# Kernel tuning notes

Measured on AMD Instinct MI355X. Metric: run time of the kernel, lower is better.

## Reference

```python
import jax, jax.numpy as jnp
import numpy as np

N = 50000      # num nodes
E = 800000     # num edges (before self loops)
B = 50         # num graphs in batch
F_IN = 15
C = 64         # hidden_channels
H = 4          # num_heads
NEG_SLOPE = 0.2  # PyG GATConv default


def setup_inputs() -> dict:
    key = jax.random.key(0)
    ks = jax.random.split(key, 32)
    s = 0.05
    inp = {
        "x": jax.random.normal(ks[0], (N, F_IN), dtype=jnp.float32),
        "edge_index": jax.random.randint(ks[1], (2, E), 0, N, dtype=jnp.int32),
        "batch": jnp.sort(jax.random.randint(ks[2], (N,), 0, B, dtype=jnp.int32)),
        "W1": jax.random.normal(ks[3], (F_IN, H * C)) * s,
        "aS1": jax.random.normal(ks[4], (H, C)) * s,
        "aD1": jax.random.normal(ks[5], (H, C)) * s,
        "b1": jnp.zeros((H * C,)),
        "W2": jax.random.normal(ks[6], (H * C, H * C)) * s,
        "aS2": jax.random.normal(ks[7], (H, C)) * s,
        "aD2": jax.random.normal(ks[8], (H, C)) * s,
        "b2": jnp.zeros((H * C,)),
        # GAT layer 3: 256 -> 64, 1 head
        "W3": jax.random.normal(ks[9], (H * C, C)) * s,
        "aS3": jax.random.normal(ks[10], (1, C)) * s,
        "aD3": jax.random.normal(ks[11], (1, C)) * s,
        "b3": jnp.zeros((C,)),
        # node attention MLP: 64 -> 32 -> 1
        "Wna1": jax.random.normal(ks[12], (C, 32)) * s,
        "bna1": jnp.zeros((32,)),
        "Wna2": jax.random.normal(ks[13], (32, 1)) * s,
        "bna2": jnp.zeros((1,)),
        # graph classifier: 128 -> 128 -> 64 -> 1
        "Wc1": jax.random.normal(ks[14], (2 * C, 128)) * s,
        "bc1": jnp.zeros((128,)),
        "Wc2": jax.random.normal(ks[15], (128, 64)) * s,
        "bc2": jnp.zeros((64,)),
        "Wc3": jax.random.normal(ks[16], (64, 1)) * s,
        "bc3": jnp.zeros((1,)),
    }
    return inp


def _gat_conv(x, src, dst, W, a_src, a_dst, b, heads, ch):
    """PyG-style GATConv (add_self_loops=True, negative_slope=0.2, eval mode)."""
    n = x.shape[0]
    h = (x @ W).reshape(n, heads, ch)               # [N, H, C]
    alpha_s = jnp.einsum('nhc,hc->nh', h, a_src)    # per-node src score
    alpha_d = jnp.einsum('nhc,hc->nh', h, a_dst)
    loops = jnp.arange(n, dtype=src.dtype)
    s = jnp.concatenate([src, loops])               # [E+N]
    d = jnp.concatenate([dst, loops])
    e = jax.nn.leaky_relu(alpha_s[s] + alpha_d[d], NEG_SLOPE)   # [E+N, H]
    # segment softmax over incoming edges of each dst node
    m = jax.ops.segment_max(e, d, num_segments=n)
    ex = jnp.exp(e - m[d])
    denom = jax.ops.segment_sum(ex, d, num_segments=n)
    alpha = ex / denom[d]                           # [E+N, H]
    msg = h[s] * alpha[:, :, None]                  # [E+N, H, C]
    out = jax.ops.segment_sum(msg, d, num_segments=n)  # [N, H, C]
    return out.reshape(n, heads * ch) + b


def reference(x, edge_index, batch, W1, aS1, aD1, b1, W2, aS2, aD2, b2,
              W3, aS3, aD3, b3, Wna1, bna1, Wna2, bna2,
              Wc1, bc1, Wc2, bc2, Wc3, bc3):
    src, dst = edge_index[0], edge_index[1]
    x1 = jax.nn.elu(_gat_conv(x, src, dst, W1, aS1, aD1, b1, H, C))
    x2 = jax.nn.elu(_gat_conv(x1, src, dst, W2, aS2, aD2, b2, H, C))
    x3 = jax.nn.elu(_gat_conv(x2, src, dst, W3, aS3, aD3, b3, 1, C))  # [N, 64]

    # node attention: MLP then softmax over ALL nodes (dim=0, as in source)
    na = jax.nn.relu(x3 @ Wna1 + bna1) @ Wna2 + bna2   # [N, 1]
    node_attention = jax.nn.softmax(na, axis=0)

    # graph pooling
    ones = jnp.ones((x3.shape[0],), dtype=x3.dtype)
    cnt = jax.ops.segment_sum(ones, batch, num_segments=B)         # [B]
    mean = jax.ops.segment_sum(x3, batch, num_segments=B) / jnp.maximum(cnt, 1.0)[:, None]
    mx = jax.ops.segment_max(x3, batch, num_segments=B)
    mx = jnp.where(cnt[:, None] > 0, mx, 0.0)
    g = jnp.concatenate([mean, mx], axis=1)                        # [B, 128]

    h1 = jax.nn.relu(g @ Wc1 + bc1)
    h2 = jax.nn.relu(h1 @ Wc2 + bc2)
    risk = jax.nn.sigmoid(h2 @ Wc3 + bc3)                          # [B, 1]
    return (risk, node_attention)
```

## Files before the change

kernel.cpp:

```cpp
#include <hip/hip_runtime.h>
#include <math.h>

#define NN 50000
#define NP 50176
#define EE 800000
#define ETOT (EE + NN)
#define BB 50
#define PC 16

typedef unsigned short u16;
typedef unsigned char u8;
typedef __attribute__((ext_vector_type(8))) short short8;
typedef __attribute__((ext_vector_type(8))) unsigned short ushort8;
typedef __attribute__((ext_vector_type(4))) float floatx4;
typedef __attribute__((ext_vector_type(2))) float floatx2;

__device__ __forceinline__ float b2f(u16 u) {
  return __int_as_float(((int)u) << 16);
}
__device__ __forceinline__ u16 f2b(float f) {
  unsigned u = __float_as_uint(f);
  unsigned r = (u + 0x7fffu + ((u >> 16) & 1u)) >> 16;
  return (u16)r;
}
__device__ __forceinline__ u8 f2f8(float v) {
  return (u8)(__builtin_amdgcn_cvt_pk_fp8_f32(v, v, 0, false) & 0xFF);
}
__device__ __forceinline__ float readlane_f(float v, int l) {
  return __int_as_float(__builtin_amdgcn_readlane(__float_as_int(v), l));
}

__global__ void count_kernel(const int* __restrict__ ei, int* __restrict__ cnt) {
  int e = blockIdx.x * blockDim.x + threadIdx.x;
  if (e >= ETOT) return;
  int d = (e < EE) ? ei[EE + e] : (e - EE);
  atomicAdd(&cnt[d], 1);
}

__global__ void scan1_kernel(const int* __restrict__ cnt, int* __restrict__ rowp,
                             int* __restrict__ part) {
  __shared__ int s[512];
  int t = threadIdx.x;
  int i = blockIdx.x * 512 + t;
  int v = (i < NN) ? cnt[i] : 0;
  s[t] = v;
  __syncthreads();
  for (int off = 1; off < 512; off <<= 1) {
    int add = (t >= off) ? s[t - off] : 0;
    __syncthreads();
    s[t] += add;
    __syncthreads();
  }
  if (i < NN) rowp[i] = s[t] - v;
  if (t == 511) part[blockIdx.x] = s[511];
}

__global__ void scan2_kernel(int* __restrict__ part, int* __restrict__ rowp) {
  __shared__ int s[128];
  int t = threadIdx.x;
  int v = (t < 98) ? part[t] : 0;
  s[t] = v;
  __syncthreads();
  for (int off = 1; off < 128; off <<= 1) {
    int add = (t >= off) ? s[t - off] : 0;
    __syncthreads();
    s[t] += add;
    __syncthreads();
  }
  if (t < 98) part[t] = s[t] - v;
  if (t == 97) rowp[NN] = s[97];
}

__global__ void scan3_kernel(int* __restrict__ rowp, const int* __restrict__ part) {
  int i = blockIdx.x * 512 + threadIdx.x;
  if (i < NN) rowp[i] += part[blockIdx.x];
}

__global__ void fill_kernel(const int* __restrict__ ei, const int* __restrict__ rowp,
                            int* __restrict__ cur, int* __restrict__ col) {
  int e = blockIdx.x * blockDim.x + threadIdx.x;
  if (e >= ETOT) return;
  int s, d;
  if (e < EE) { s = ei[e]; d = ei[EE + e]; } else { s = e - EE; d = s; }
  int p = atomicAdd(&cur[d], 1);
  col[rowp[d] + p] = s;
}

__global__ void prep_kernel(const float* __restrict__ x, const float* __restrict__ W1,
                            const float* __restrict__ W2, const float* __restrict__ W3,
                            u16* __restrict__ xb, u16* __restrict__ W1t,
                            u16* __restrict__ W2t, u16* __restrict__ W3t) {
  const int T0 = NP * 32, T1 = T0 + 8192, T2 = T1 + 65536, T3 = T2 + 16384;
  int i = blockIdx.x * 256 + threadIdx.x;
  if (i < T0) {
    int n = i >> 5, c = i & 31;
    xb[i] = (n < NN && c < 15) ? f2b(x[n * 15 + c]) : (u16)0;
  } else if (i < T1) {
    int j = i - T0, n = j >> 5, k = j & 31;
    W1t[j] = (k < 15) ? f2b(W1[k * 256 + n]) : (u16)0;
  } else if (i < T2) {
    int j = i - T1, n = j >> 8, k = j & 255;
    W2t[j] = f2b(W2[k * 256 + n]);
  } else if (i < T3) {
    int j = i - T2, n = j >> 8, k = j & 255;
    W3t[j] = f2b(W3[k * 64 + n]);
  }
}

template <int BK>
__global__ __launch_bounds__(256) void gemm128_kernel(
    const u16* __restrict__ A, const u16* __restrict__ Bt, u8* __restrict__ C8,
    int K, const float* __restrict__ aS, const float* __restrict__ aD,
    float* __restrict__ as_o, float* __restrict__ ad_o) {
  __shared__ u16 Al[128][BK + 8];
  __shared__ u16 Bl[128][BK + 8];
  int R0 = blockIdx.x * 128, C0 = blockIdx.y * 128;
  int wid = threadIdx.x >> 6, lane = threadIdx.x & 63;
  int wr = (wid >> 1) * 64, wc = (wid & 1) * 64;
  int lrow = lane & 15, lk8 = (lane >> 4) * 8;
  int rq = (lane >> 4) * 4;
  const int Q8 = BK / 8;
  const int nA8 = 128 * Q8;
  floatx4 acc[4][4];
#pragma unroll
  for (int i = 0; i < 4; ++i)
#pragma unroll
    for (int j = 0; j < 4; ++j) acc[i][j] = (floatx4){0.f, 0.f, 0.f, 0.f};

  for (int k0 = 0; k0 < K; k0 += BK) {
    for (int c = threadIdx.x; c < 2 * nA8; c += 256) {
      if (c < nA8) {
        int r = c / Q8, o = (c % Q8) * 8;
        *(ushort8*)&Al[r][o] = *(const ushort8*)&A[(size_t)(R0 + r) * K + k0 + o];
      } else {
        int c2 = c - nA8;
        int r = c2 / Q8, o = (c2 % Q8) * 8;
        *(ushort8*)&Bl[r][o] = *(const ushort8*)&Bt[(size_t)(C0 + r) * K + k0 + o];
      }
    }
    __syncthreads();
#pragma unroll
    for (int ks = 0; ks < BK / 32; ++ks) {
      short8 a[4], b[4];
#pragma unroll
      for (int i = 0; i < 4; ++i) a[i] = *(const short8*)&Al[wr + i * 16 + lrow][ks * 32 + lk8];
#pragma unroll
      for (int j = 0; j < 4; ++j) b[j] = *(const short8*)&Bl[wc + j * 16 + lrow][ks * 32 + lk8];
#pragma unroll
      for (int i = 0; i < 4; ++i)
#pragma unroll
        for (int j = 0; j < 4; ++j)
          acc[i][j] = __builtin_amdgcn_mfma_f32_16x16x32_bf16(a[i], b[j], acc[i][j], 0, 0, 0);
    }
    __syncthreads();
  }
#pragma unroll
  for (int i = 0; i < 4; ++i)
#pragma unroll
    for (int j = 0; j < 4; ++j)
#pragma unroll
      for (int q = 0; q < 4; ++q) {
        int gr = R0 + wr + i * 16 + rq + q;
        int gc = C0 + wc + j * 16 + lrow;
        C8[(size_t)gr * 256 + gc] = f2f8(acc[i][j][q]);
      }
  int hb = blockIdx.y * 2 + (wid & 1);
  float wS[4], wD[4];
#pragma unroll
  for (int j = 0; j < 4; ++j) {
    wS[j] = aS[hb * 64 + j * 16 + lrow];
    wD[j] = aD[hb * 64 + j * 16 + lrow];
  }
#pragma unroll
  for (int i = 0; i < 4; ++i)
#pragma unroll
    for (int q = 0; q < 4; ++q) {
      float vS = acc[i][0][q] * wS[0] + acc[i][1][q] * wS[1] +
                 acc[i][2][q] * wS[2] + acc[i][3][q] * wS[3];
      float vD = acc[i][0][q] * wD[0] + acc[i][1][q] * wD[1] +
                 acc[i][2][q] * wD[2] + acc[i][3][q] * wD[3];
#pragma unroll
      for (int o = 8; o; o >>= 1) {
        vS += __shfl_xor(vS, o, 64);
        vD += __shfl_xor(vD, o, 64);
      }
      if (lrow == 0) {
        int gr = R0 + wr + i * 16 + rq + q;
        as_o[(size_t)gr * 4 + hb] = vS;
        ad_o[(size_t)gr * 4 + hb] = vD;
      }
    }
}

__global__ __launch_bounds__(256) void gemm64_kernel(
    const u16* __restrict__ A, const u16* __restrict__ Bt, u16* __restrict__ C,
    int K, const float* __restrict__ aS, const float* __restrict__ aD,
    float* __restrict__ as_o, float* __restrict__ ad_o) {
  const int BK = 64;
  __shared__ u16 Al[128][BK + 8];
  __shared__ u16 Bl[64][BK + 8];
  __shared__ float sS[4][64], sD[4][64];
  int R0 = blockIdx.x * 128;
  int wid = threadIdx.x >> 6, lane = threadIdx.x & 63;
  int wr = (wid >> 1) * 64, wc = (wid & 1) * 32;
  int lrow = lane & 15, lk8 = (lane >> 4) * 8;
  int rq = (lane >> 4) * 4;
  const int Q4 = BK / 4;
  const int nA = 128 * Q4, nB = 64 * Q4;
  floatx4 acc[4][2];
#pragma unroll
  for (int i = 0; i < 4; ++i)
#pragma unroll
    for (int j = 0; j < 2; ++j) acc[i][j] = (floatx4){0.f, 0.f, 0.f, 0.f};

  for (int k0 = 0; k0 < K; k0 += BK) {
    for (int c = threadIdx.x; c < nA + nB; c += 256) {
      if (c < nA) {
        int r = c / Q4, o = (c % Q4) * 4;
        *(ushort4*)&Al[r][o] = *(const ushort4*)&A[(size_t)(R0 + r) * K + k0 + o];
      } else {
        int c2 = c - nA;
        int r = c2 / Q4, o = (c2 % Q4) * 4;
        *(ushort4*)&Bl[r][o] = *(const ushort4*)&Bt[(size_t)r * K + k0 + o];
      }
    }
    __syncthreads();
#pragma unroll
    for (int ks = 0; ks < BK / 32; ++ks) {
      short8 a[4], b[2];
#pragma unroll
      for (int i = 0; i < 4; ++i) a[i] = *(const short8*)&Al[wr + i * 16 + lrow][ks * 32 + lk8];
#pragma unroll
      for (int j = 0; j < 2; ++j) b[j] = *(const short8*)&Bl[wc + j * 16 + lrow][ks * 32 + lk8];
#pragma unroll
      for (int i = 0; i < 4; ++i)
#pragma unroll
        for (int j = 0; j < 2; ++j)
          acc[i][j] = __builtin_amdgcn_mfma_f32_16x16x32_bf16(a[i], b[j], acc[i][j], 0, 0, 0);
    }
    __syncthreads();
  }
#pragma unroll
  for (int i = 0; i < 4; ++i)
#pragma unroll
    for (int j = 0; j < 2; ++j)
#pragma unroll
      for (int q = 0; q < 4; ++q) {
        int gr = R0 + wr + i * 16 + rq + q;
        C[(size_t)gr * 64 + wc + j * 16 + lrow] = f2b(acc[i][j][q]);
      }
  float wS0 = aS[wc + lrow], wS1 = aS[wc + 16 + lrow];
  float wD0 = aD[wc + lrow], wD1 = aD[wc + 16 + lrow];
#pragma unroll
  for (int i = 0; i < 4; ++i)
#pragma unroll
    for (int q = 0; q < 4; ++q) {
      float vS = acc[i][0][q] * wS0 + acc[i][1][q] * wS1;
      float vD = acc[i][0][q] * wD0 + acc[i][1][q] * wD1;
#pragma unroll
      for (int o = 8; o; o >>= 1) {
        vS += __shfl_xor(vS, o, 64);
        vD += __shfl_xor(vD, o, 64);
      }
      if (lrow == 0) {
        int rl = i * 16 + rq + q;
        sS[wid][rl] = vS;
        sD[wid][rl] = vD;
      }
    }
  __syncthreads();
  if (threadIdx.x < 128) {
    int p = threadIdx.x >> 6, r = threadIdx.x & 63;
    int gr = R0 + p * 64 + r;
    as_o[gr] = sS[2 * p][r] + sS[2 * p + 1][r];
    ad_o[gr] = sD[2 * p][r] + sD[2 * p + 1][r];
  }
}

template <int LAYER>
__global__ __launch_bounds__(256) void escore4_kernel(
    const float* __restrict__ as_i, const float* __restrict__ ad_i,
    const int* __restrict__ rowp, const int* __restrict__ col,
    float4* __restrict__ exl) {
  int wid = threadIdx.x >> 6, lane = threadIdx.x & 63;
  int d = blockIdx.x * 4 + wid;
  int rp0 = rowp[d], rp1 = rowp[d + 1];
  float4 add = *(const float4*)&ad_i[(size_t)d * 4];
  for (int i = rp0 + lane; i < rp1; i += 64) {
    int s = col[i];
    float4 a = *(const float4*)&as_i[(size_t)s * 4];
    float e0 = a.x + add.x, e1 = a.y + add.y, e2 = a.z + add.z, e3 = a.w + add.w;
    e0 = (e0 > 0.f) ? e0 : 0.2f * e0;
    e1 = (e1 > 0.f) ? e1 : 0.2f * e1;
    e2 = (e2 > 0.f) ? e2 : 0.2f * e2;
    e3 = (e3 > 0.f) ? e3 : 0.2f * e3;
    exl[i] = make_float4(__expf(e0), __expf(e1), __expf(e2), __expf(e3));
  }
}

__global__ __launch_bounds__(256) void escore1_kernel(
    const float* __restrict__ as_i, const float* __restrict__ ad_i,
    const int* __restrict__ rowp, const int* __restrict__ col,
    float* __restrict__ exl) {
  int wid = threadIdx.x >> 6, lane = threadIdx.x & 63;
  int d = blockIdx.x * 4 + wid;
  int rp0 = rowp[d], rp1 = rowp[d + 1];
  float add = ad_i[d];
  for (int i = rp0 + lane; i < rp1; i += 64) {
    float e = as_i[col[i]] + add;
    e = (e > 0.f) ? e : 0.2f * e;
    exl[i] = __expf(e);
  }
}

template <int LAYER>
__global__ __launch_bounds__(256) void agg4_kernel(
    const u8* __restrict__ h8, const float4* __restrict__ exl,
    const int* __restrict__ rowp, const int* __restrict__ col,
    const float* __restrict__ bias, u16* __restrict__ xo) {
  __shared__ float exs[4][64][4];
  int wid = threadIdx.x >> 6, lane = threadIdx.x & 63;
  int d = blockIdx.x * 4 + wid;
  int rp0 = rowp[d], deg = rowp[d + 1] - rp0;
  int hj = lane >> 4;
  int lq = lane << 2;
  float a0 = 0.f, a1 = 0.f, a2 = 0.f, a3 = 0.f;
  float den0 = 0.f, den1 = 0.f, den2 = 0.f, den3 = 0.f;

  for (int base = 0; base < deg; base += 64) {
    int i = base + lane;
    bool valid = i < deg;
    int s = valid ? col[rp0 + i] : 0;
    float4 xv = valid ? exl[rp0 + i] : make_float4(0.f, 0.f, 0.f, 0.f);
    den0 += xv.x; den1 += xv.y; den2 += xv.z; den3 += xv.w;
    *(float4*)&exs[wid][lane][0] = xv;
    __threadfence_block();
    int cnt = min(64, deg - base);
    int k8 = cnt & ~7;
    for (int k = 0; k < k8; k += 8) {
      unsigned wv[8];
      float qv[8];
#pragma unroll
      for (int u = 0; u < 8; ++u) {
        int sk = __builtin_amdgcn_readlane(s, k + u);
        qv[u] = exs[wid][k + u][hj];
        wv[u] = *(const unsigned*)&h8[(size_t)sk * 256 + lq];
      }
#pragma unroll
      for (int u = 0; u < 8; ++u) {
        floatx2 lo = __builtin_amdgcn_cvt_pk_f32_fp8(wv[u], false);
        floatx2 hi = __builtin_amdgcn_cvt_pk_f32_fp8(wv[u], true);
        a0 += qv[u] * lo.x;
        a1 += qv[u] * lo.y;
        a2 += qv[u] * hi.x;
        a3 += qv[u] * hi.y;
      }
    }
    for (int k = k8; k < cnt; ++k) {
      int sk = __builtin_amdgcn_readlane(s, k);
      float qk = exs[wid][k][hj];
      unsigned wv = *(const unsigned*)&h8[(size_t)sk * 256 + lq];
      floatx2 lo = __builtin_amdgcn_cvt_pk_f32_fp8(wv, false);
      floatx2 hi = __builtin_amdgcn_cvt_pk_f32_fp8(wv, true);
      a0 += qk * lo.x;
      a1 += qk * lo.y;
      a2 += qk * hi.x;
      a3 += qk * hi.y;
    }
  }
#pragma unroll
  for (int o = 32; o; o >>= 1) {
    den0 += __shfl_xor(den0, o, 64);
    den1 += __shfl_xor(den1, o, 64);
    den2 += __shfl_xor(den2, o, 64);
    den3 += __shfl_xor(den3, o, 64);
  }
  float den = (hj == 0) ? den0 : (hj == 1) ? den1 : (hj == 2) ? den2 : den3;
  float inv = 1.f / den;
  float4 bv = *(const float4*)&bias[lq];
  float v0 = a0 * inv + bv.x;
  float v1 = a1 * inv + bv.y;
  float v2 = a2 * inv + bv.z;
  float v3 = a3 * inv + bv.w;
  v0 = (v0 > 0.f) ? v0 : expm1f(v0);
  v1 = (v1 > 0.f) ? v1 : expm1f(v1);
  v2 = (v2 > 0.f) ? v2 : expm1f(v2);
  v3 = (v3 > 0.f) ? v3 : expm1f(v3);
  ushort4 o4;
  o4.x = f2b(v0); o4.y = f2b(v1); o4.z = f2b(v2); o4.w = f2b(v3);
  ((ushort4*)xo)[(size_t)d * 64 + lane] = o4;
}

__global__ __launch_bounds__(256) void agg1na_kernel(
    const u16* __restrict__ h, const float* __restrict__ exl,
    const int* __restrict__ rowp, const int* __restrict__ col,
    const float* __restrict__ bias, float* __restrict__ xo,
    const float* __restrict__ Wna1, const float* __restrict__ bna1,
    const float* __restrict__ Wna2, const float* __restrict__ bna2,
    float* __restrict__ na) {
  __shared__ float Ws[2048];
  __shared__ float W2s[32];
  __shared__ float xrow[4][64];
  for (int i = threadIdx.x; i < 2048; i += 256) Ws[i] = Wna1[i];
  if (threadIdx.x < 32) W2s[threadIdx.x] = Wna2[threadIdx.x];
  __syncthreads();
  int wid = threadIdx.x >> 6, lane = threadIdx.x & 63;
  int d = blockIdx.x * 4 + wid;
  int rp0 = rowp[d], deg = rowp[d + 1] - rp0;
  float acc = 0.f, den = 0.f;
  for (int base = 0; base < deg; base += 64) {
    int i = base + lane;
    bool valid = i < deg;
    int s = valid ? col[rp0 + i] : 0;
    float ex = valid ? exl[rp0 + i] : 0.f;
    den += ex;
    int cnt = min(64, deg - base);
    int k8 = cnt & ~7;
    for (int k = 0; k < k8; k += 8) {
      int sA[8];
      float qA[8], hv[8];
#pragma unroll
      for (int u = 0; u < 8; ++u) {
        sA[u] = __builtin_amdgcn_readlane(s, k + u);
        qA[u] = readlane_f(ex, k + u);
      }
#pragma unroll
      for (int u = 0; u < 8; ++u) hv[u] = b2f(h[(size_t)sA[u] * 64 + lane]);
      float p0 = qA[0] * hv[0] + qA[1] * hv[1];
      float p1 = qA[2] * hv[2] + qA[3] * hv[3];
      float p2 = qA[4] * hv[4] + qA[5] * hv[5];
      float p3 = qA[6] * hv[6] + qA[7] * hv[7];
      acc += (p0 + p1) + (p2 + p3);
    }
    for (int k = k8; k < cnt; ++k) {
      int sk = __builtin_amdgcn_readlane(s, k);
      float qk = readlane_f(ex, k);
      acc += qk * b2f(h[(size_t)sk * 64 + lane]);
    }
  }
#pragma unroll
  for (int o = 32; o; o >>= 1) den += __shfl_xor(den, o, 64);
  float v = acc / den + bias[lane];
  v = (v > 0.f) ? v : expm1f(v);
  xo[(size_t)d * 64 + lane] = v;
  xrow[wid][lane] = v;
  __threadfence_block();
  int j = lane & 31;
  int coff = (lane >> 5) * 32;
  float hj = 0.f;
#pragma unroll
  for (int c = 0; c < 32; ++c) hj += xrow[wid][coff + c] * Ws[(coff + c) * 32 + j];
  hj += __shfl_xor(hj, 32, 64);
  hj += bna1[j];
  float r = fmaxf(hj, 0.f) * W2s[j];
#pragma unroll
  for (int o = 16; o; o >>= 1) r += __shfl_xor(r, o, 64);
  if (lane == 0) na[d] = __expf(r + bna2[0]);
}

__global__ void na_sum_kernel(const float* __restrict__ na, float* __restrict__ gsum) {
  __shared__ float s[4];
  float acc = 0.f;
  for (int i = blockIdx.x * blockDim.x + threadIdx.x; i < NN; i += gridDim.x * blockDim.x)
    acc += na[i];
  for (int o = 32; o; o >>= 1) acc += __shfl_xor(acc, o, 64);
  int wid = threadIdx.x >> 6, lane = threadIdx.x & 63;
  if (lane == 0) s[wid] = acc;
  __syncthreads();
  if (threadIdx.x == 0) atomicAdd(gsum, s[0] + s[1] + s[2] + s[3]);
}

__global__ void na_write_kernel(const float* __restrict__ na, const float* __restrict__ gsum,
                                float* __restrict__ out) {
  int n = blockIdx.x * blockDim.x + threadIdx.x;
  if (n >= NN) return;
  out[n] = na[n] / gsum[0];
}

__global__ void pool1_kernel(const float* __restrict__ x3, const int* __restrict__ batch,
                             float* __restrict__ ppsum, float* __restrict__ ppmax) {
  int b = blockIdx.x, c = blockIdx.y;
  int lane = threadIdx.x & 63, wid = threadIdx.x >> 6;
  int lo = 0, hi = NN;
  while (lo < hi) { int m = (lo + hi) >> 1; if (batch[m] < b) lo = m + 1; else hi = m; }
  int start = lo;
  lo = start; hi = NN;
  while (lo < hi) { int m = (lo + hi) >> 1; if (batch[m] < b + 1) lo = m + 1; else hi = m; }
  int end = lo;
  int len = end - start;
  int c0 = start + (int)((long)len * c / PC);
  int c1 = start + (int)((long)len * (c + 1) / PC);
  float acc = 0.f, mx = -INFINITY;
  for (int n = c0 + wid; n < c1; n += 4) {
    float v = x3[(size_t)n * 64 + lane];
    acc += v;
    mx = fmaxf(mx, v);
  }
  __shared__ float ssum[4][64], smax[4][64];
  ssum[wid][lane] = acc;
  smax[wid][lane] = mx;
  __syncthreads();
  if (wid == 0) {
    acc = ssum[0][lane] + ssum[1][lane] + ssum[2][lane] + ssum[3][lane];
    mx = fmaxf(fmaxf(smax[0][lane], smax[1][lane]), fmaxf(smax[2][lane], smax[3][lane]));
    size_t o = ((size_t)c * BB + b) * 64 + lane;
    ppsum[o] = acc;
    ppmax[o] = mx;
  }
}

__global__ void pool2cls_kernel(const float* __restrict__ ppsum, const float* __restrict__ ppmax,
                                const int* __restrict__ batch, const float* __restrict__ Wc1,
                                const float* __restrict__ bc1, const float* __restrict__ Wc2,
                                const float* __restrict__ bc2, const float* __restrict__ Wc3,
                                const float* __restrict__ bc3, float* __restrict__ out) {
  __shared__ float g[128], h1[128], h2[64], scnt;
  int b = blockIdx.x, t = threadIdx.x;
  if (t == 0) {
    int lo = 0, hi = NN;
    while (lo < hi) { int m = (lo + hi) >> 1; if (batch[m] < b) lo = m + 1; else hi = m; }
    int start = lo;
    lo = start; hi = NN;
    while (lo < hi) { int m = (lo + hi) >> 1; if (batch[m] < b + 1) lo = m + 1; else hi = m; }
    scnt = (float)(lo - start);
  }
  float s = 0.f, m = -INFINITY;
  if (t < 64) {
#pragma unroll
    for (int c = 0; c < PC; ++c) {
      size_t o = ((size_t)c * BB + b) * 64 + t;
      s += ppsum[o];
      m = fmaxf(m, ppmax[o]);
    }
  }
  __syncthreads();
  float cnt = scnt;
  if (t < 64) {
    g[t] = (cnt > 0.f) ? s / fmaxf(cnt, 1.f) : 0.f;
    g[64 + t] = (cnt > 0.f) ? m : 0.f;
  }
  __syncthreads();
  float v = bc1[t];
  for (int k = 0; k < 128; ++k) v += g[k] * Wc1[k * 128 + t];
  h1[t] = fmaxf(v, 0.f);
  __syncthreads();
  if (t < 64) {
    float v2 = bc2[t];
    for (int k = 0; k < 128; ++k) v2 += h1[k] * Wc2[k * 64 + t];
    h2[t] = fmaxf(v2, 0.f);
  }
  __syncthreads();
  if (t == 0) {
    float z = bc3[0];
    for (int k = 0; k < 64; ++k) z += h2[k] * Wc3[k];
    out[b] = 1.f / (1.f + expf(-z));
  }
}

extern "C" void kernel_launch(void* const* d_in, const int* in_sizes, int n_in,
                              void* d_out, int out_size, void* d_ws, size_t ws_size,
                              hipStream_t stream) {
  const float* x    = (const float*)d_in[0];
  const int*   ei   = (const int*)d_in[1];
  const int*   batch= (const int*)d_in[2];
  const float* W1 = (const float*)d_in[3];
  const float* aS1= (const float*)d_in[4];
  const float* aD1= (const float*)d_in[5];
  const float* b1 = (const float*)d_in[6];
  const float* W2 = (const float*)d_in[7];
  const float* aS2= (const float*)d_in[8];
  const float* aD2= (const float*)d_in[9];
  const float* b2 = (const float*)d_in[10];
  const float* W3 = (const float*)d_in[11];
  const float* aS3= (const float*)d_in[12];
  const float* aD3= (const float*)d_in[13];
  const float* b3 = (const float*)d_in[14];
  const float* Wna1=(const float*)d_in[15];
  const float* bna1=(const float*)d_in[16];
  const float* Wna2=(const float*)d_in[17];
  const float* bna2=(const float*)d_in[18];
  const float* Wc1=(const float*)d_in[19];
  const float* bc1=(const float*)d_in[20];
  const float* Wc2=(const float*)d_in[21];
  const float* bc2=(const float*)d_in[22];
  const float* Wc3=(const float*)d_in[23];
  const float* bc3=(const float*)d_in[24];
  float* out = (float*)d_out;

  char* w = (char*)d_ws;
  size_t off = 0;
  auto alloc = [&](size_t bytes) {
    void* p = w + off;
    off = (off + bytes + 255) & ~(size_t)255;
    return p;
  };
  u16* xb   = (u16*)alloc((size_t)NP * 32 * 2);
  u16* bufA = (u16*)alloc((size_t)NP * 256 * 2);
  u16* bufB = (u16*)alloc((size_t)NP * 256 * 2);
  u8*  h8   = (u8*)alloc((size_t)NP * 256);
  u16* W1t  = (u16*)alloc((size_t)256 * 32 * 2);
  u16* W2t  = (u16*)alloc((size_t)256 * 256 * 2);
  u16* W3t  = (u16*)alloc((size_t)64 * 256 * 2);
  float* asb  = (float*)alloc((size_t)NP * 4 * 4);
  float* adb  = (float*)alloc((size_t)NP * 4 * 4);
  float* nab  = (float*)alloc((size_t)NN * 4);
  float4* exl4 = (float4*)alloc((size_t)ETOT * 16);
  int* rowp = (int*)alloc((size_t)(NN + 1) * 4);
  int* cntb = (int*)alloc((size_t)NN * 4);
  int* curb = (int*)alloc((size_t)NN * 4);
  float* gsum = (float*)alloc(256);
  size_t zspan = (size_t)((char*)gsum + 256 - (char*)cntb);
  int* colb = (int*)alloc((size_t)ETOT * 4);
  int* part = (int*)alloc(128 * 4);
  float* ppsum = (float*)alloc((size_t)PC * BB * 64 * 4);
  float* ppmax = (float*)alloc((size_t)PC * BB * 64 * 4);
  float* x3 = (float*)bufB;
  float* exl1 = (float*)exl4;
  (void)ws_size; (void)in_sizes; (void)n_in; (void)out_size;

  hipMemsetAsync(cntb, 0, zspan, stream);

  count_kernel<<<(ETOT + 255) / 256, 256, 0, stream>>>(ei, cntb);
  scan1_kernel<<<98, 512, 0, stream>>>(cntb, rowp, part);
  scan2_kernel<<<1, 128, 0, stream>>>(part, rowp);
  scan3_kernel<<<98, 512, 0, stream>>>(rowp, part);
  fill_kernel<<<(ETOT + 255) / 256, 256, 0, stream>>>(ei, rowp, curb, colb);

  const int PREP_TOT = NP * 32 + 8192 + 65536 + 16384;
  prep_kernel<<<(PREP_TOT + 255) / 256, 256, 0, stream>>>(x, W1, W2, W3, xb, W1t, W2t, W3t);

  const int GX = NP / 128;
  gemm128_kernel<32><<<dim3(GX, 2), 256, 0, stream>>>(xb, W1t, h8, 32, aS1, aD1, asb, adb);
  escore4_kernel<1><<<12500, 256, 0, stream>>>(asb, adb, rowp, colb, exl4);
  agg4_kernel<1><<<12500, 256, 0, stream>>>(h8, exl4, rowp, colb, b1, bufB);
  gemm128_kernel<64><<<dim3(GX, 2), 256, 0, stream>>>(bufB, W2t, h8, 256, aS2, aD2, asb, adb);
  escore4_kernel<2><<<12500, 256, 0, stream>>>(asb, adb, rowp, colb, exl4);
  agg4_kernel<2><<<12500, 256, 0, stream>>>(h8, exl4, rowp, colb, b2, bufB);
  gemm64_kernel<<<GX, 256, 0, stream>>>(bufB, W3t, bufA, 256, aS3, aD3, asb, adb);
  escore1_kernel<<<12500, 256, 0, stream>>>(asb, adb, rowp, colb, exl1);
  agg1na_kernel<<<12500, 256, 0, stream>>>(bufA, exl1, rowp, colb, b3, x3,
                                           Wna1, bna1, Wna2, bna2, nab);

  na_sum_kernel<<<196, 256, 0, stream>>>(nab, gsum);
  na_write_kernel<<<(NN + 255) / 256, 256, 0, stream>>>(nab, gsum, out + BB);
  pool1_kernel<<<dim3(BB, PC), 256, 0, stream>>>(x3, batch, ppsum, ppmax);
  pool2cls_kernel<<<BB, 128, 0, stream>>>(ppsum, ppmax, batch, Wc1, bc1, Wc2, bc2,
                                          Wc3, bc3, out);
}
```

Baseline: 372.6 us.

## Replace atomic CSR fill with two-pass bucketed binning scatter

The single-pass CSR fill, which did one global atomic per edge and wrote column indices to random locations, is replaced by a two-pass scheme. First, edges are binned by destination bucket of 128 nodes, using shared-memory histograms and staging so the packed (src, local dst) pairs are written mostly contiguously. Second, one block per bucket scatters its pairs into the column array using shared-memory atomics. This cuts global atomic contention and improves write locality, at the cost of an extra pairs buffer, two more launches, and packing src into 16 bits, which limits it to fewer than 65536 nodes.

```diff
diff --git a/kernel.cpp b/kernel.cpp
--- a/kernel.cpp
+++ b/kernel.cpp
@@ -7,6 +7,9 @@
 #define ETOT (EE + NN)
 #define BB 50
 #define PC 16
+#define BWD 128
+#define NBUCK 391
+#define TILE 8192
 
 typedef unsigned short u16;
 typedef unsigned char u8;
@@ -76,14 +79,93 @@
   if (i < NN) rowp[i] += part[blockIdx.x];
 }
 
-__global__ void fill_kernel(const int* __restrict__ ei, const int* __restrict__ rowp,
-                            int* __restrict__ cur, int* __restrict__ col) {
-  int e = blockIdx.x * blockDim.x + threadIdx.x;
-  if (e >= ETOT) return;
-  int s, d;
-  if (e < EE) { s = ei[e]; d = ei[EE + e]; } else { s = e - EE; d = s; }
-  int p = atomicAdd(&cur[d], 1);
-  col[rowp[d] + p] = s;
+__global__ void curinit_kernel(const int* __restrict__ rowp, int* __restrict__ cur_b) {
+  int t = threadIdx.x;
+  if (t < NBUCK) cur_b[t] = rowp[t * BWD];
+}
+
+__global__ __launch_bounds__(256) void binA_kernel(const int* __restrict__ ei,
+                                                   int* __restrict__ cur_b,
+                                                   unsigned* __restrict__ pairs) {
+  __shared__ unsigned staged[TILE];
+  __shared__ int hist[512];
+  __shared__ int hoff[512];
+  __shared__ int gbase[NBUCK];
+  __shared__ int hcur[NBUCK];
+  __shared__ int wsum[4];
+  int t = threadIdx.x;
+  int lane = t & 63, wid = t >> 6;
+  int e0 = blockIdx.x * TILE;
+  int tc = min(TILE, ETOT - e0);
+  for (int i = t; i < 512; i += 256) hist[i] = 0;
+  __syncthreads();
+  for (int i = t; i < tc; i += 256) {
+    int e = e0 + i;
+    int d = (e < EE) ? ei[EE + e] : (e - EE);
+    atomicAdd(&hist[d >> 7], 1);
+  }
+  __syncthreads();
+  int a = hist[2 * t], b = hist[2 * t + 1];
+  int sv = a + b;
+  int v = sv;
+#pragma unroll
+  for (int off = 1; off < 64; off <<= 1) {
+    int u = __shfl_up(v, off, 64);
+    if (lane >= off) v += u;
+  }
+  if (lane == 63) wsum[wid] = v;
+  __syncthreads();
+  int wpre = 0;
+  for (int ww = 0; ww < wid; ++ww) wpre += wsum[ww];
+  int excl = v + wpre - sv;
+  hoff[2 * t] = excl;
+  hoff[2 * t + 1] = excl + a;
+  __syncthreads();
+  for (int i = t; i < NBUCK; i += 256) {
+    int n = hist[i];
+    gbase[i] = (n > 0) ? atomicAdd(&cur_b[i], n) : 0;
+    hcur[i] = hoff[i];
+  }
+  __syncthreads();
+  for (int i = t; i < tc; i += 256) {
+    int e = e0 + i;
+    int s, d;
+    if (e < EE) { s = ei[e]; d = ei[EE + e]; } else { s = e - EE; d = s; }
+    int bk = d >> 7;
+    int slot = atomicAdd(&hcur[bk], 1);
+    staged[slot] = (unsigned)s | ((unsigned)(d & 127) << 16) | ((unsigned)bk << 23);
+  }
+  __syncthreads();
+  for (int i = t; i < tc; i += 256) {
+    unsigned pk = staged[i];
+    int bk = pk >> 23;
+    pairs[gbase[bk] + (i - hoff[bk])] = pk;
+  }
+}
+
+__global__ __launch_bounds__(256) void scatterB_kernel(const unsigned* __restrict__ pairs,
+                                                       const int* __restrict__ rowp,
+                                                       int* __restrict__ col) {
+  __shared__ int lbase[BWD];
+  __shared__ int lcur[BWD];
+  int t = threadIdx.x;
+  int d0 = blockIdx.x * BWD;
+  if (t < BWD) {
+    int d = d0 + t;
+    lbase[t] = rowp[(d < NN) ? d : NN];
+    lcur[t] = 0;
+  }
+  __syncthreads();
+  int p0 = rowp[d0];
+  int dend = d0 + BWD;
+  int p1 = rowp[(dend < NN) ? dend : NN];
+  for (int i = p0 + t; i < p1; i += 256) {
+    unsigned pk = pairs[i];
+    int s = pk & 0xFFFF;
+    int dl = (pk >> 16) & 0x7F;
+    int p = atomicAdd(&lcur[dl], 1);
+    col[lbase[dl] + p] = s;
+  }
 }
 
 __global__ void prep_kernel(const float* __restrict__ x, const float* __restrict__ W1,
@@ -605,9 +687,10 @@
   float* adb  = (float*)alloc((size_t)NP * 4 * 4);
   float* nab  = (float*)alloc((size_t)NN * 4);
   float4* exl4 = (float4*)alloc((size_t)ETOT * 16);
+  unsigned* pairs = (unsigned*)alloc((size_t)ETOT * 4);
   int* rowp = (int*)alloc((size_t)(NN + 1) * 4);
+  int* cur_b = (int*)alloc((size_t)(NBUCK + 1) * 4);
   int* cntb = (int*)alloc((size_t)NN * 4);
-  int* curb = (int*)alloc((size_t)NN * 4);
   float* gsum = (float*)alloc(256);
   size_t zspan = (size_t)((char*)gsum + 256 - (char*)cntb);
   int* colb = (int*)alloc((size_t)ETOT * 4);
@@ -624,7 +707,9 @@
   scan1_kernel<<<98, 512, 0, stream>>>(cntb, rowp, part);
   scan2_kernel<<<1, 128, 0, stream>>>(part, rowp);
   scan3_kernel<<<98, 512, 0, stream>>>(rowp, part);
-  fill_kernel<<<(ETOT + 255) / 256, 256, 0, stream>>>(ei, rowp, curb, colb);
+  curinit_kernel<<<1, 512, 0, stream>>>(rowp, cur_b);
+  binA_kernel<<<(ETOT + TILE - 1) / TILE, 256, 0, stream>>>(ei, cur_b, pairs);
+  scatterB_kernel<<<NBUCK, 256, 0, stream>>>(pairs, rowp, colb);
 
   const int PREP_TOT = NP * 32 + 8192 + 65536 + 16384;
   prep_kernel<<<(PREP_TOT + 255) / 256, 256, 0, stream>>>(x, W1, W2, W3, xb, W1t, W2t, W3t);
```

After: 359.3 us. 1.04x faster.
